# Optimization experiments

Hardware: AMD Instinct MI355X
Metric: run time of the kernel (lower is better)

Reference implementation:

```python
import jax, jax.numpy as jnp
import numpy as np

EMBED = 1024
HEADS = 16
HEAD_DIM = EMBED // HEADS
HIDDEN = 4 * EMBED
EPS = 1e-5


def setup_inputs() -> dict:
    key = jax.random.key(0)
    ks = jax.random.split(key, 9)
    s = lambda fan_in: 1.0 / np.sqrt(fan_in)
    inp = {
        "x": jax.random.normal(ks[0], (2, 2048, EMBED), dtype=jnp.float32),
        "ln1_w": jnp.ones((EMBED,), jnp.float32),
        "ln1_b": jnp.zeros((EMBED,), jnp.float32),
        "ln2_w": jnp.ones((EMBED,), jnp.float32),
        "ln2_b": jnp.zeros((EMBED,), jnp.float32),
        "qkv_w": jax.random.uniform(ks[1], (EMBED, 3 * EMBED), jnp.float32, -s(EMBED), s(EMBED)),
        "qkv_b": jax.random.uniform(ks[2], (3 * EMBED,), jnp.float32, -s(EMBED), s(EMBED)),
        "proj_w": jax.random.uniform(ks[3], (EMBED, EMBED), jnp.float32, -s(EMBED), s(EMBED)),
        "proj_b": jax.random.uniform(ks[4], (EMBED,), jnp.float32, -s(EMBED), s(EMBED)),
        "fc1_w": jax.random.uniform(ks[5], (EMBED, HIDDEN), jnp.float32, -s(EMBED), s(EMBED)),
        "fc1_b": jax.random.uniform(ks[6], (HIDDEN,), jnp.float32, -s(EMBED), s(EMBED)),
        "fc2_w": jax.random.uniform(ks[7], (HIDDEN, EMBED), jnp.float32, -s(HIDDEN), s(HIDDEN)),
        "fc2_b": jax.random.uniform(ks[8], (EMBED,), jnp.float32, -s(HIDDEN), s(HIDDEN)),
    }
    return inp


def _layernorm(x, w, b):
    mu = jnp.mean(x, axis=-1, keepdims=True)
    var = jnp.mean(jnp.square(x - mu), axis=-1, keepdims=True)
    return (x - mu) * jax.lax.rsqrt(var + EPS) * w + b


def _attn(x, qkv_w, qkv_b, proj_w, proj_b):
    B, N, C = x.shape
    qkv = x @ qkv_w + qkv_b                      # [B,N,3C]
    qkv = qkv.reshape(B, N, 3, HEADS, HEAD_DIM)
    q, k, v = qkv[:, :, 0], qkv[:, :, 1], qkv[:, :, 2]   # [B,N,H,D]
    scale = HEAD_DIM ** -0.5
    scores = jnp.einsum("bqhd,bkhd->bhqk", q, k) * scale  # [B,H,N,N]
    attn = jax.nn.softmax(scores, axis=-1)
    out = jnp.einsum("bhqk,bkhd->bqhd", attn, v).reshape(B, N, C)
    return out @ proj_w + proj_b


def _mlp(x, fc1_w, fc1_b, fc2_w, fc2_b):
    h = jax.nn.gelu(x @ fc1_w + fc1_b, approximate=False)
    return h @ fc2_w + fc2_b


def reference(x, ln1_w, ln1_b, ln2_w, ln2_b, qkv_w, qkv_b, proj_w, proj_b,
              fc1_w, fc1_b, fc2_w, fc2_b):
    # pre-norm transformer block (eval mode: dropout/drop_path are identity)
    x = x + _attn(_layernorm(x, ln1_w, ln1_b), qkv_w, qkv_b, proj_w, proj_b)
    x = x + _mlp(_layernorm(x, ln2_w, ln2_b), fc1_w, fc1_b, fc2_w, fc2_b)
    return x
```

## Files before the change

kernel.cpp:

```cpp
#include <hip/hip_runtime.h>
#include <hip/hip_bf16.h>

#define SEQ    2048
#define BATCH  2
#define MTOK   4096
#define EMBED  1024
#define HEADS  16
#define HDIM   64
#define QKV3   3072
#define FFN    4096

typedef __attribute__((ext_vector_type(8))) short bf16x8;
typedef __attribute__((ext_vector_type(4))) float f32x4;
typedef __attribute__((ext_vector_type(16))) float f32x16;

static __device__ __forceinline__ unsigned short f2bf(float f) {
  union { float f; unsigned u; } x; x.f = f;
  unsigned r = x.u + 0x7FFFu + ((x.u >> 16) & 1u);
  return (unsigned short)(r >> 16);
}
static __device__ __forceinline__ float bf2f(unsigned short u) {
  union { unsigned u; float f; } x; x.u = ((unsigned)u) << 16; return x.f;
}
static __device__ __forceinline__ unsigned pk2bf(float a, float b) {
#if __has_builtin(__builtin_amdgcn_cvt_pk_bf16_f32)
  typedef __attribute__((ext_vector_type(2))) __bf16 bf16x2_t;
  union { bf16x2_t v; unsigned u; } x;
  x.v = __builtin_amdgcn_cvt_pk_bf16_f32(a, b);
  return x.u;
#else
  return ((unsigned)f2bf(a)) | (((unsigned)f2bf(b)) << 16);
#endif
}
static __device__ __forceinline__ float fexp2(float x) {
#if __has_builtin(__builtin_amdgcn_exp2f)
  return __builtin_amdgcn_exp2f(x);
#else
  return exp2f(x);
#endif
}
static __device__ __forceinline__ float frcp(float x) {
#if __has_builtin(__builtin_amdgcn_rcpf)
  return __builtin_amdgcn_rcpf(x);
#else
  return 1.0f / x;
#endif
}
static __device__ __forceinline__ float fgelu(float v) {
  float t = v * v;
  float z = v * __builtin_fmaf(-0.1029456f, t, -2.3022650687f);
  return v * frcp(1.0f + fexp2(z));
}

static __device__ __forceinline__ void gload16(const unsigned short* g, unsigned short* l) {
  __builtin_amdgcn_global_load_lds((const __attribute__((address_space(1))) void*)g,
                                   (__attribute__((address_space(3))) void*)l, 16, 0, 0);
}

struct TD { const float* W; unsigned short* T; int K, N, ntx, base; };
struct TD4 { TD d[4]; };

__global__ void transpose_all(TD4 td) {
  __shared__ float t[32][33];
  int bid = blockIdx.x;
  int i = 0;
  if (bid >= td.d[1].base) i = 1;
  if (bid >= td.d[2].base) i = 2;
  if (bid >= td.d[3].base) i = 3;
  const TD& D = td.d[i];
  int local = bid - D.base;
  int n0 = (local % D.ntx) * 32, k0 = (local / D.ntx) * 32;
  int tx = threadIdx.x, ty = threadIdx.y;
#pragma unroll
  for (int j = 0; j < 32; j += 8)
    t[ty + j][tx] = D.W[(size_t)(k0 + ty + j) * D.N + n0 + tx];
  __syncthreads();
#pragma unroll
  for (int j = 0; j < 32; j += 8)
    D.T[(size_t)(n0 + ty + j) * D.K + k0 + tx] = f2bf(t[tx][ty + j]);
}

__global__ __launch_bounds__(256) void ln_kernel(const float* __restrict__ in,
                                                 const float* __restrict__ w,
                                                 const float* __restrict__ b,
                                                 unsigned short* __restrict__ out) {
  __shared__ float sh[4];
  int row = blockIdx.x, tid = threadIdx.x;
  const float4 v = ((const float4*)(in + (size_t)row * EMBED))[tid];
  float s = v.x + v.y + v.z + v.w;
#pragma unroll
  for (int off = 32; off; off >>= 1) s += __shfl_xor(s, off);
  if ((tid & 63) == 0) sh[tid >> 6] = s;
  __syncthreads();
  float mean = (sh[0] + sh[1] + sh[2] + sh[3]) * (1.0f / EMBED);
  __syncthreads();
  float dx = v.x - mean, dy = v.y - mean, dz = v.z - mean, dw = v.w - mean;
  float q = dx * dx + dy * dy + dz * dz + dw * dw;
#pragma unroll
  for (int off = 32; off; off >>= 1) q += __shfl_xor(q, off);
  if ((tid & 63) == 0) sh[tid >> 6] = q;
  __syncthreads();
  float var = (sh[0] + sh[1] + sh[2] + sh[3]) * (1.0f / EMBED);
  float rs = rsqrtf(var + 1e-5f);
  const float4 wv = ((const float4*)w)[tid];
  const float4 bv = ((const float4*)b)[tid];
  ushort4 o;
  o.x = f2bf(dx * rs * wv.x + bv.x);
  o.y = f2bf(dy * rs * wv.y + bv.y);
  o.z = f2bf(dz * rs * wv.z + bv.z);
  o.w = f2bf(dw * rs * wv.w + bv.w);
  ((ushort4*)(out + (size_t)row * EMBED))[tid] = o;
}

template <int ACT, int OUTBF, int VSPLIT>
__global__ __launch_bounds__(256) void gemmBig(const unsigned short* __restrict__ A,
                                               const unsigned short* __restrict__ Wt,
                                               const float* __restrict__ bias,
                                               unsigned short* __restrict__ outB,
                                               float* __restrict__ outF,
                                               unsigned short* __restrict__ vT,
                                               int M, int N, int K, int nblk) {
  __shared__ __align__(16) unsigned short As[128 * 64];
  __shared__ __align__(16) unsigned short Bs[128 * 64];
  const int tid = threadIdx.x;
  const int wave = tid >> 6, lane = tid & 63;
  const int quad = lane >> 4, ml = lane & 15;
  const int wr = wave >> 1, wc = wave & 1;
  const int m0 = (blockIdx.x / nblk) * 128;
  const int n0 = (blockIdx.x % nblk) * 128;
  const int srow = lane >> 3;
  const int schunk = (lane & 7) ^ (srow & 7);
  const unsigned short* Ag = A + (size_t)(m0 + wave * 32 + srow) * K + schunk * 8;
  const unsigned short* Bg = Wt + (size_t)(n0 + wave * 32 + srow) * K + schunk * 8;
  unsigned short* AsW = &As[wave * 2048];
  unsigned short* BsW = &Bs[wave * 2048];
  f32x4 acc[4][4];
#pragma unroll
  for (int i = 0; i < 4; i++)
#pragma unroll
    for (int j = 0; j < 4; j++) acc[i][j] = (f32x4){0.f, 0.f, 0.f, 0.f};
  for (int k0 = 0; k0 < K; k0 += 64) {
    __syncthreads();
#pragma unroll
    for (int t = 0; t < 4; t++) {
      gload16(Ag + (size_t)(8 * t) * K, AsW + 512 * t);
      gload16(Bg + (size_t)(8 * t) * K, BsW + 512 * t);
    }
    Ag += 64; Bg += 64;
    __syncthreads();
#pragma unroll
    for (int kh = 0; kh < 2; kh++) {
      const int ch = ((kh * 4 + quad) ^ (ml & 7)) * 8;
      bf16x8 af[4], bfr[4];
#pragma unroll
      for (int mt = 0; mt < 4; mt++)
        af[mt] = *(const bf16x8*)&As[(wr * 64 + mt * 16 + ml) * 64 + ch];
#pragma unroll
      for (int nt = 0; nt < 4; nt++)
        bfr[nt] = *(const bf16x8*)&Bs[(wc * 64 + nt * 16 + ml) * 64 + ch];
#pragma unroll
      for (int mt = 0; mt < 4; mt++)
#pragma unroll
        for (int nt = 0; nt < 4; nt++)
          acc[mt][nt] = __builtin_amdgcn_mfma_f32_16x16x32_bf16(af[mt], bfr[nt], acc[mt][nt], 0, 0, 0);
    }
  }
#pragma unroll
  for (int mt = 0; mt < 4; mt++)
#pragma unroll
    for (int nt = 0; nt < 4; nt++) {
      const int col0 = n0 + wc * 64 + nt * 16;
      const int row0 = m0 + wr * 64 + mt * 16;
      if (VSPLIT && col0 >= 2 * EMBED) {
        const int b = row0 >> 11, tok0 = row0 & (SEQ - 1);
        const int h = (col0 - 2 * EMBED) >> 6;
        const int dl = ((col0 - 2 * EMBED) & 63) + ml;
        float bia = bias[col0 + ml];
        ushort4 o;
        o.x = f2bf(acc[mt][nt][0] + bia);
        o.y = f2bf(acc[mt][nt][1] + bia);
        o.z = f2bf(acc[mt][nt][2] + bia);
        o.w = f2bf(acc[mt][nt][3] + bia);
        *(ushort4*)(vT + (size_t)((b * 16 + h) * 64 + dl) * SEQ + tok0 + quad * 4) = o;
      } else {
#pragma unroll
        for (int r = 0; r < 4; r++) {
          int row = row0 + quad * 4 + r;
          int col = col0 + ml;
          float v = acc[mt][nt][r] + bias[col];
          if (ACT) v = fgelu(v);
          if (OUTBF)
            outB[(size_t)row * N + col] = f2bf(v);
          else
            outF[(size_t)row * N + col] = v;
        }
      }
    }
}

template <int RES, int OUTBF>
__global__ __launch_bounds__(256) void gemm64k(const unsigned short* __restrict__ A,
                                               const unsigned short* __restrict__ Wt,
                                               const float* __restrict__ bias,
                                               const float* __restrict__ res,
                                               unsigned short* __restrict__ outB,
                                               float* __restrict__ outF,
                                               int M, int N, int K, int nblk) {
  __shared__ __align__(16) unsigned short As[2][128 * 64];
  __shared__ __align__(16) unsigned short Bs[2][64 * 64];
  const int tid = threadIdx.x;
  const int wave = tid >> 6, lane = tid & 63;
  const int quad = lane >> 4, ml = lane & 15;
  const int wr = wave >> 1, wc = wave & 1;
  const int xcd = blockIdx.x & 7, idx = blockIdx.x >> 3;
  const int mPerXcd = (gridDim.x >> 3) / nblk;
  const int m0 = (xcd * mPerXcd + idx / nblk) * 128;
  const int n0 = (idx % nblk) * 64;
  const int srow = lane >> 3;
  const int schunk = (lane & 7) ^ (srow & 7);
  const unsigned short* Ag = A + (size_t)(m0 + wave * 32 + srow) * K + schunk * 8;
  const unsigned short* Bg = Wt + (size_t)(n0 + wave * 16 + srow) * K + schunk * 8;
  f32x4 acc[4][2];
#pragma unroll
  for (int i = 0; i < 4; i++) { acc[i][0] = (f32x4){0.f,0.f,0.f,0.f}; acc[i][1] = acc[i][0]; }
  {
    unsigned short* AsW = &As[0][wave * 2048];
    unsigned short* BsW = &Bs[0][wave * 1024];
    gload16(Ag, AsW);
    gload16(Ag + (size_t)8 * K,  AsW + 512);
    gload16(Ag + (size_t)16 * K, AsW + 1024);
    gload16(Ag + (size_t)24 * K, AsW + 1536);
    gload16(Bg, BsW);
    gload16(Bg + (size_t)8 * K,  BsW + 512);
    Ag += 64; Bg += 64;
  }
  __syncthreads();
  const int nk = K >> 6;
  for (int kk = 0; kk < nk; ++kk) {
    const int cur = kk & 1;
    if (kk + 1 < nk) {
      unsigned short* AsW = &As[cur ^ 1][wave * 2048];
      unsigned short* BsW = &Bs[cur ^ 1][wave * 1024];
      gload16(Ag, AsW);
      gload16(Ag + (size_t)8 * K,  AsW + 512);
      gload16(Ag + (size_t)16 * K, AsW + 1024);
      gload16(Ag + (size_t)24 * K, AsW + 1536);
      gload16(Bg, BsW);
      gload16(Bg + (size_t)8 * K,  BsW + 512);
      Ag += 64; Bg += 64;
    }
#pragma unroll
    for (int kh = 0; kh < 2; kh++) {
      const int ch = ((kh * 4 + quad) ^ (ml & 7)) * 8;
      bf16x8 af[4], bfr[2];
#pragma unroll
      for (int mt = 0; mt < 4; mt++)
        af[mt] = *(const bf16x8*)&As[cur][(wr * 64 + mt * 16 + ml) * 64 + ch];
#pragma unroll
      for (int nt = 0; nt < 2; nt++)
        bfr[nt] = *(const bf16x8*)&Bs[cur][(wc * 32 + nt * 16 + ml) * 64 + ch];
#pragma unroll
      for (int mt = 0; mt < 4; mt++)
#pragma unroll
        for (int nt = 0; nt < 2; nt++)
          acc[mt][nt] = __builtin_amdgcn_mfma_f32_16x16x32_bf16(af[mt], bfr[nt], acc[mt][nt], 0, 0, 0);
    }
    __syncthreads();
  }
#pragma unroll
  for (int mt = 0; mt < 4; mt++)
#pragma unroll
    for (int nt = 0; nt < 2; nt++)
#pragma unroll
      for (int r = 0; r < 4; r++) {
        int row = m0 + wr * 64 + mt * 16 + quad * 4 + r;
        int col = n0 + wc * 32 + nt * 16 + ml;
        float v = acc[mt][nt][r] + bias[col];
        if (RES) v += res[(size_t)row * N + col];
        if (OUTBF)
          outB[(size_t)row * N + col] = f2bf(v);
        else
          outF[(size_t)row * N + col] = v;
      }
}

__global__ __launch_bounds__(256, 2) void attn_kernel(const unsigned short* __restrict__ qkv,
                                                      const unsigned short* __restrict__ vT,
                                                      unsigned short* __restrict__ attn) {
  __shared__ __align__(16) unsigned short Ks[2][64 * 64];
  __shared__ __align__(16) unsigned short Vs[2][64 * 64];
  const int tid = threadIdx.x, wave = tid >> 6, lane = tid & 63;
  const int l31 = lane & 31, hi = lane >> 5;
  const int bh = blockIdx.x, b = bh >> 4, h = bh & 15;
  const int q0w = blockIdx.y * 128 + wave * 32;
  const float qscale = 0.18033688011112042f;
  const int sw = l31 & 7;

  const unsigned short* qrow = qkv + (size_t)(b * SEQ + q0w + l31) * QKV3 + h * HDIM;
  bf16x8 bq[4];
#pragma unroll
  for (int s = 0; s < 4; s++) {
    bq[s] = *(const bf16x8*)(qrow + s * 16 + hi * 8);
#pragma unroll
    for (int j = 0; j < 8; j++)
      bq[s][j] = (short)f2bf(bf2f((unsigned short)bq[s][j]) * qscale);
  }
  bf16x8 ones;
#pragma unroll
  for (int j = 0; j < 8; j++) ones[j] = (short)0x3F80;

  f32x16 zz;
#pragma unroll
  for (int i = 0; i < 16; i++) zz[i] = 0.f;
  f32x16 O0 = zz, O1 = zz, lsum = zz;

  const int skey = lane >> 3;
  const int schunk8 = ((lane & 7) ^ (skey & 7)) * 8;
  const unsigned short* kbase =
      qkv + (size_t)(b * SEQ + wave * 16 + skey) * QKV3 + EMBED + h * HDIM + schunk8;
  const unsigned short* vbase =
      vT + (size_t)(bh * 64 + wave * 16 + skey) * SEQ + schunk8;

  gload16(kbase, &Ks[0][wave * 1024]);
  gload16(kbase + (size_t)8 * QKV3, &Ks[0][wave * 1024] + 512);
  gload16(vbase, &Vs[0][wave * 1024]);
  gload16(vbase + (size_t)8 * SEQ, &Vs[0][wave * 1024] + 512);
  __syncthreads();

  for (int kti = 0; kti < SEQ / 64; ++kti) {
    const int cur = kti & 1;
    if (kti + 1 < SEQ / 64) {
      const int kt = (kti + 1) * 64;
      unsigned short* kd = &Ks[cur ^ 1][wave * 1024];
      unsigned short* vd = &Vs[cur ^ 1][wave * 1024];
      gload16(kbase + (size_t)kt * QKV3, kd);
      gload16(kbase + (size_t)(kt + 8) * QKV3, kd + 512);
      gload16(vbase + kt, vd);
      gload16(vbase + kt + (size_t)8 * SEQ, vd + 512);
    }
    const unsigned short* Kc = &Ks[cur][0];
    const unsigned short* Vc = &Vs[cur][0];

    f32x16 St0 = zz, St1 = zz;
#pragma unroll
    for (int s = 0; s < 4; s++) {
      bf16x8 ak0 = *(const bf16x8*)&Kc[l31 * 64 + (((2 * s + hi) ^ sw)) * 8];
      bf16x8 ak1 = *(const bf16x8*)&Kc[(32 + l31) * 64 + (((2 * s + hi) ^ sw)) * 8];
      St0 = __builtin_amdgcn_mfma_f32_32x32x16_bf16(ak0, bq[s], St0, 0, 0, 0);
      St1 = __builtin_amdgcn_mfma_f32_32x32x16_bf16(ak1, bq[s], St1, 0, 0, 0);
    }

    unsigned W0[2][4], W1[2][4];
#pragma unroll
    for (int g = 0; g < 4; g++) {
      W0[0][g] = pk2bf(fexp2(St0[4 * g]), fexp2(St0[4 * g + 1]));
      W1[0][g] = pk2bf(fexp2(St0[4 * g + 2]), fexp2(St0[4 * g + 3]));
      W0[1][g] = pk2bf(fexp2(St1[4 * g]), fexp2(St1[4 * g + 1]));
      W1[1][g] = pk2bf(fexp2(St1[4 * g + 2]), fexp2(St1[4 * g + 3]));
    }

    bf16x8 pa[4];
#pragma unroll
    for (int ks = 0; ks < 4; ks++) {
      const int kt2 = ks >> 1, g0 = 2 * (ks & 1), g1 = g0 + 1;
      unsigned send0 = hi ? W0[kt2][g0] : W0[kt2][g1];
      unsigned send1 = hi ? W1[kt2][g0] : W1[kt2][g1];
      unsigned recv0 = __shfl_xor((int)send0, 32);
      unsigned recv1 = __shfl_xor((int)send1, 32);
      union { unsigned u[4]; bf16x8 v; } pw;
      pw.u[0] = hi ? recv0 : W0[kt2][g0];
      pw.u[1] = hi ? recv1 : W1[kt2][g0];
      pw.u[2] = hi ? W0[kt2][g1] : recv0;
      pw.u[3] = hi ? W1[kt2][g1] : recv1;
      pa[ks] = pw.v;
    }

    __builtin_amdgcn_s_setprio(1);
#pragma unroll
    for (int ks = 0; ks < 4; ks++)
      lsum = __builtin_amdgcn_mfma_f32_32x32x16_bf16(pa[ks], ones, lsum, 0, 0, 0);
#pragma unroll
    for (int ks = 0; ks < 4; ks++) {
      bf16x8 bv0 = *(const bf16x8*)&Vc[l31 * 64 + (((2 * ks + hi) ^ sw)) * 8];
      bf16x8 bv1 = *(const bf16x8*)&Vc[(32 + l31) * 64 + (((2 * ks + hi) ^ sw)) * 8];
      O0 = __builtin_amdgcn_mfma_f32_32x32x16_bf16(pa[ks], bv0, O0, 0, 0, 0);
      O1 = __builtin_amdgcn_mfma_f32_32x32x16_bf16(pa[ks], bv1, O1, 0, 0, 0);
    }
    __builtin_amdgcn_s_setprio(0);
    __syncthreads();
  }

#pragma unroll
  for (int r = 0; r < 16; r++) {
    const int qr = (r & 3) + 8 * (r >> 2) + 4 * hi;
    float inv = 1.0f / lsum[r];
    size_t g = (size_t)(b * SEQ + q0w + qr) * EMBED + h * HDIM + l31;
    attn[g]      = f2bf(O0[r] * inv);
    attn[g + 32] = f2bf(O1[r] * inv);
  }
}

extern "C" void kernel_launch(void* const* d_in, const int* in_sizes, int n_in,
                              void* d_out, int out_size, void* d_ws, size_t ws_size,
                              hipStream_t stream) {
  const float* x      = (const float*)d_in[0];
  const float* ln1_w  = (const float*)d_in[1];
  const float* ln1_b  = (const float*)d_in[2];
  const float* ln2_w  = (const float*)d_in[3];
  const float* ln2_b  = (const float*)d_in[4];
  const float* qkv_w  = (const float*)d_in[5];
  const float* qkv_b  = (const float*)d_in[6];
  const float* proj_w = (const float*)d_in[7];
  const float* proj_b = (const float*)d_in[8];
  const float* fc1_w  = (const float*)d_in[9];
  const float* fc1_b  = (const float*)d_in[10];
  const float* fc2_w  = (const float*)d_in[11];
  const float* fc2_b  = (const float*)d_in[12];
  float* out = (float*)d_out;
  char* wsb = (char*)d_ws;
  unsigned short* lnbuf  = (unsigned short*)(wsb + 0);
  unsigned short* qkvb   = (unsigned short*)(wsb + 8388608);
  unsigned short* attnb  = (unsigned short*)(wsb + 33554432);
  unsigned short* vTb    = (unsigned short*)(wsb + 41943040);
  unsigned short* actb   = (unsigned short*)(wsb + 33554432);
  float*          h1     = (float*)(wsb + 67108864);
  unsigned short* qkvWt  = (unsigned short*)(wsb + 83886080);
  unsigned short* projWt = (unsigned short*)(wsb + 90177536);
  unsigned short* fc1Wt  = (unsigned short*)(wsb + 92274688);
  unsigned short* fc2Wt  = (unsigned short*)(wsb + 100663296);

  TD4 td;
  td.d[0] = {qkv_w,  qkvWt,  1024, 3072,  96, 0};
  td.d[1] = {proj_w, projWt, 1024, 1024,  32, 3072};
  td.d[2] = {fc1_w,  fc1Wt,  1024, 4096, 128, 4096};
  td.d[3] = {fc2_w,  fc2Wt,  4096, 1024,  32, 8192};
  transpose_all<<<12288, dim3(32, 8), 0, stream>>>(td);

  ln_kernel<<<MTOK, 256, 0, stream>>>(x, ln1_w, ln1_b, lnbuf);
  gemmBig<0, 1, 1><<<768, 256, 0, stream>>>(
      lnbuf, qkvWt, qkv_b, qkvb, nullptr, vTb, MTOK, QKV3, EMBED, 24);
  attn_kernel<<<dim3(32, 16), 256, 0, stream>>>(qkvb, vTb, attnb);
  gemm64k<1, 0><<<512, 256, 0, stream>>>(
      attnb, projWt, proj_b, x, nullptr, h1, MTOK, EMBED, EMBED, 16);
  ln_kernel<<<MTOK, 256, 0, stream>>>(h1, ln2_w, ln2_b, lnbuf);
  gemmBig<1, 1, 0><<<1024, 256, 0, stream>>>(
      lnbuf, fc1Wt, fc1_b, actb, nullptr, nullptr, MTOK, FFN, EMBED, 32);
  gemm64k<1, 0><<<512, 256, 0, stream>>>(
      actb, fc2Wt, fc2_b, h1, nullptr, out, MTOK, EMBED, FFN, 16);
}
```

Before: 366.1 us.

## Split attention key tiles across wave pairs and reduce partial outputs in LDS

The attention kernel now has each block cover 64 queries with 4 waves. Pairs of waves share a 32-query slice and each wave handles half of every 64-key tile. Their partial row sums and outputs are combined through shared memory at the end. This doubles the grid to 1024 blocks and raises the occupancy hint, to fill more CUs and cut per-wave MFMA serial work. It also replaces the shuffle-based P-fragment exchange with permlane32_swap when that builtin is available. In exchange, each K/V tile is loaded for half as many queries, and there is an extra LDS reduction and sync.

```diff
diff --git a/kernel.cpp b/kernel.cpp
--- a/kernel.cpp
+++ b/kernel.cpp
@@ -50,6 +50,21 @@
   float t = v * v;
   float z = v * __builtin_fmaf(-0.1029456f, t, -2.3022650687f);
   return v * frcp(1.0f + fexp2(z));
+}
+
+static __device__ __forceinline__ void halfswap(unsigned a, unsigned b, int hi,
+                                                unsigned& lo_out, unsigned& hi_out) {
+#if __has_builtin(__builtin_amdgcn_permlane32_swap)
+  typedef __attribute__((ext_vector_type(2))) unsigned uint2v;
+  uint2v r = __builtin_amdgcn_permlane32_swap(a, b, false, false);
+  lo_out = r[0];
+  hi_out = r[1];
+#else
+  unsigned as = (unsigned)__shfl_xor((int)a, 32);
+  unsigned bs = (unsigned)__shfl_xor((int)b, 32);
+  lo_out = hi ? bs : a;
+  hi_out = hi ? b : as;
+#endif
 }
 
 static __device__ __forceinline__ void gload16(const unsigned short* g, unsigned short* l) {
@@ -284,15 +299,16 @@
       }
 }
 
-__global__ __launch_bounds__(256, 2) void attn_kernel(const unsigned short* __restrict__ qkv,
+__global__ __launch_bounds__(256, 4) void attn_kernel(const unsigned short* __restrict__ qkv,
                                                       const unsigned short* __restrict__ vT,
                                                       unsigned short* __restrict__ attn) {
   __shared__ __align__(16) unsigned short Ks[2][64 * 64];
   __shared__ __align__(16) unsigned short Vs[2][64 * 64];
   const int tid = threadIdx.x, wave = tid >> 6, lane = tid & 63;
   const int l31 = lane & 31, hi = lane >> 5;
+  const int qs = wave & 1, kh = wave >> 1;
   const int bh = blockIdx.x, b = bh >> 4, h = bh & 15;
-  const int q0w = blockIdx.y * 128 + wave * 32;
+  const int q0w = blockIdx.y * 64 + qs * 32;
   const float qscale = 0.18033688011112042f;
   const int sw = l31 & 7;
 
@@ -327,6 +343,7 @@
   gload16(vbase + (size_t)8 * SEQ, &Vs[0][wave * 1024] + 512);
   __syncthreads();
 
+  const int krow0 = kh * 32;
   for (int kti = 0; kti < SEQ / 64; ++kti) {
     const int cur = kti & 1;
     if (kti + 1 < SEQ / 64) {
@@ -341,48 +358,40 @@
     const unsigned short* Kc = &Ks[cur][0];
     const unsigned short* Vc = &Vs[cur][0];
 
-    f32x16 St0 = zz, St1 = zz;
+    f32x16 St = zz;
 #pragma unroll
     for (int s = 0; s < 4; s++) {
-      bf16x8 ak0 = *(const bf16x8*)&Kc[l31 * 64 + (((2 * s + hi) ^ sw)) * 8];
-      bf16x8 ak1 = *(const bf16x8*)&Kc[(32 + l31) * 64 + (((2 * s + hi) ^ sw)) * 8];
-      St0 = __builtin_amdgcn_mfma_f32_32x32x16_bf16(ak0, bq[s], St0, 0, 0, 0);
-      St1 = __builtin_amdgcn_mfma_f32_32x32x16_bf16(ak1, bq[s], St1, 0, 0, 0);
-    }
-
-    unsigned W0[2][4], W1[2][4];
+      bf16x8 ak = *(const bf16x8*)&Kc[(krow0 + l31) * 64 + ((2 * s + hi) ^ sw) * 8];
+      St = __builtin_amdgcn_mfma_f32_32x32x16_bf16(ak, bq[s], St, 0, 0, 0);
+    }
+
+    unsigned W0[4], W1[4];
 #pragma unroll
     for (int g = 0; g < 4; g++) {
-      W0[0][g] = pk2bf(fexp2(St0[4 * g]), fexp2(St0[4 * g + 1]));
-      W1[0][g] = pk2bf(fexp2(St0[4 * g + 2]), fexp2(St0[4 * g + 3]));
-      W0[1][g] = pk2bf(fexp2(St1[4 * g]), fexp2(St1[4 * g + 1]));
-      W1[1][g] = pk2bf(fexp2(St1[4 * g + 2]), fexp2(St1[4 * g + 3]));
-    }
-
-    bf16x8 pa[4];
-#pragma unroll
-    for (int ks = 0; ks < 4; ks++) {
-      const int kt2 = ks >> 1, g0 = 2 * (ks & 1), g1 = g0 + 1;
-      unsigned send0 = hi ? W0[kt2][g0] : W0[kt2][g1];
-      unsigned send1 = hi ? W1[kt2][g0] : W1[kt2][g1];
-      unsigned recv0 = __shfl_xor((int)send0, 32);
-      unsigned recv1 = __shfl_xor((int)send1, 32);
+      W0[g] = pk2bf(fexp2(St[4 * g]), fexp2(St[4 * g + 1]));
+      W1[g] = pk2bf(fexp2(St[4 * g + 2]), fexp2(St[4 * g + 3]));
+    }
+
+    bf16x8 pa[2];
+#pragma unroll
+    for (int ks = 0; ks < 2; ks++) {
+      const int g0 = 2 * ks, g1 = g0 + 1;
+      unsigned w0, w1, w2, w3;
+      halfswap(W0[g0], W0[g1], hi, w0, w2);
+      halfswap(W1[g0], W1[g1], hi, w1, w3);
       union { unsigned u[4]; bf16x8 v; } pw;
-      pw.u[0] = hi ? recv0 : W0[kt2][g0];
-      pw.u[1] = hi ? recv1 : W1[kt2][g0];
-      pw.u[2] = hi ? W0[kt2][g1] : recv0;
-      pw.u[3] = hi ? W1[kt2][g1] : recv1;
+      pw.u[0] = w0; pw.u[1] = w1; pw.u[2] = w2; pw.u[3] = w3;
       pa[ks] = pw.v;
     }
 
     __builtin_amdgcn_s_setprio(1);
-#pragma unroll
-    for (int ks = 0; ks < 4; ks++)
-      lsum = __builtin_amdgcn_mfma_f32_32x32x16_bf16(pa[ks], ones, lsum, 0, 0, 0);
-#pragma unroll
-    for (int ks = 0; ks < 4; ks++) {
-      bf16x8 bv0 = *(const bf16x8*)&Vc[l31 * 64 + (((2 * ks + hi) ^ sw)) * 8];
-      bf16x8 bv1 = *(const bf16x8*)&Vc[(32 + l31) * 64 + (((2 * ks + hi) ^ sw)) * 8];
+    lsum = __builtin_amdgcn_mfma_f32_32x32x16_bf16(pa[0], ones, lsum, 0, 0, 0);
+    lsum = __builtin_amdgcn_mfma_f32_32x32x16_bf16(pa[1], ones, lsum, 0, 0, 0);
+#pragma unroll
+    for (int ks = 0; ks < 2; ks++) {
+      const int ch = kh * 4 + ks * 2 + hi;
+      bf16x8 bv0 = *(const bf16x8*)&Vc[l31 * 64 + (ch ^ sw) * 8];
+      bf16x8 bv1 = *(const bf16x8*)&Vc[(32 + l31) * 64 + (ch ^ sw) * 8];
       O0 = __builtin_amdgcn_mfma_f32_32x32x16_bf16(pa[ks], bv0, O0, 0, 0, 0);
       O1 = __builtin_amdgcn_mfma_f32_32x32x16_bf16(pa[ks], bv1, O1, 0, 0, 0);
     }
@@ -390,13 +399,32 @@
     __syncthreads();
   }
 
-#pragma unroll
-  for (int r = 0; r < 16; r++) {
-    const int qr = (r & 3) + 8 * (r >> 2) + 4 * hi;
-    float inv = 1.0f / lsum[r];
-    size_t g = (size_t)(b * SEQ + q0w + qr) * EMBED + h * HDIM + l31;
-    attn[g]      = f2bf(O0[r] * inv);
-    attn[g + 32] = f2bf(O1[r] * inv);
+  if (kh == 1) {
+    float* sc = qs ? (float*)&Vs[0][0] : (float*)&Ks[0][0];
+#pragma unroll
+    for (int r = 0; r < 16; r++) {
+      sc[lane * 48 + r]      = lsum[r];
+      sc[lane * 48 + 16 + r] = O0[r];
+      sc[lane * 48 + 32 + r] = O1[r];
+    }
+  }
+  __syncthreads();
+  if (kh == 0) {
+    const float* sc = qs ? (const float*)&Vs[0][0] : (const float*)&Ks[0][0];
+#pragma unroll
+    for (int r = 0; r < 16; r++) {
+      lsum[r] += sc[lane * 48 + r];
+      O0[r]   += sc[lane * 48 + 16 + r];
+      O1[r]   += sc[lane * 48 + 32 + r];
+    }
+#pragma unroll
+    for (int r = 0; r < 16; r++) {
+      const int qr = (r & 3) + 8 * (r >> 2) + 4 * hi;
+      float inv = 1.0f / lsum[r];
+      size_t g = (size_t)(b * SEQ + q0w + qr) * EMBED + h * HDIM + l31;
+      attn[g]      = f2bf(O0[r] * inv);
+      attn[g + 32] = f2bf(O1[r] * inv);
+    }
   }
 }
 
@@ -439,7 +467,7 @@
   ln_kernel<<<MTOK, 256, 0, stream>>>(x, ln1_w, ln1_b, lnbuf);
   gemmBig<0, 1, 1><<<768, 256, 0, stream>>>(
       lnbuf, qkvWt, qkv_b, qkvb, nullptr, vTb, MTOK, QKV3, EMBED, 24);
-  attn_kernel<<<dim3(32, 16), 256, 0, stream>>>(qkvb, vTb, attnb);
+  attn_kernel<<<dim3(32, 32), 256, 0, stream>>>(qkvb, vTb, attnb);
   gemm64k<1, 0><<<512, 256, 0, stream>>>(
       attnb, projWt, proj_b, x, nullptr, h1, MTOK, EMBED, EMBED, 16);
   ln_kernel<<<MTOK, 256, 0, stream>>>(h1, ln2_w, ln2_b, lnbuf);
```

Result: faster. 343.5 us (-6.2%).
